# Kernel tuning notes

Hardware: AMD Instinct MI355X
Metric: run time of the kernel (lower is better)

## Reference

```python
import jax, jax.numpy as jnp
import numpy as np

N_HEADS = 16
GROUP_SIZE = 4
D_MODEL = 2048
N_GROUPS = N_HEADS // GROUP_SIZE  # 4 KV heads
HEAD_DIM = D_MODEL // N_HEADS     # 128
B, S = 2, 2048


def setup_inputs() -> dict:
    key = jax.random.key(0)
    ks = jax.random.split(key, 10)
    sd = 1.0 / np.sqrt(D_MODEL)
    inp = {
        "x": jax.random.normal(ks[0], (B, S, D_MODEL), dtype=jnp.float32),
        # per-position, per-pair rotation angles (llama-style freqs)
        "rotary_freqs": jax.random.uniform(ks[1], (S, HEAD_DIM // 2), dtype=jnp.float32) * 6.283,
        # weights stored as [in, out] so forward is x @ W + b
        "Wq": jax.random.normal(ks[2], (D_MODEL, D_MODEL), dtype=jnp.float32) * sd,
        "bq": jnp.zeros((D_MODEL,), dtype=jnp.float32),
        "Wk": jax.random.normal(ks[3], (D_MODEL, N_GROUPS * HEAD_DIM), dtype=jnp.float32) * sd,
        "bk": jnp.zeros((N_GROUPS * HEAD_DIM,), dtype=jnp.float32),
        "Wv": jax.random.normal(ks[4], (D_MODEL, N_GROUPS * HEAD_DIM), dtype=jnp.float32) * sd,
        "bv": jnp.zeros((N_GROUPS * HEAD_DIM,), dtype=jnp.float32),
        "Wo": jax.random.normal(ks[5], (D_MODEL, D_MODEL), dtype=jnp.float32) * sd,
        "bo": jnp.zeros((D_MODEL,), dtype=jnp.float32),
    }
    return inp


def _rope(t, cos, sin):
    # t: [B, S, H, head_dim]; cos/sin: [1, S, 1, head_dim//2]
    t2 = t.reshape(t.shape[:-1] + (HEAD_DIM // 2, 2))
    te, to = t2[..., 0], t2[..., 1]
    re = te * cos - to * sin
    ro = te * sin + to * cos
    return jnp.stack([re, ro], axis=-1).reshape(t.shape)


def reference(x, rotary_freqs, Wq, bq, Wk, bk, Wv, bv, Wo, bo):
    Bx, Sx, _ = x.shape
    q = (x @ Wq + bq).reshape(Bx, Sx, N_HEADS, HEAD_DIM)
    k = (x @ Wk + bk).reshape(Bx, Sx, N_GROUPS, HEAD_DIM)
    v = (x @ Wv + bv).reshape(Bx, Sx, N_GROUPS, HEAD_DIM)

    cos = jnp.cos(rotary_freqs)[None, :, None, :]
    sin = jnp.sin(rotary_freqs)[None, :, None, :]
    q = _rope(q, cos, sin)
    k = _rope(k, cos, sin)

    q = q.transpose(0, 2, 1, 3)  # [B, H, S, hd]
    k = k.transpose(0, 2, 1, 3)  # [B, G, S, hd]
    v = v.transpose(0, 2, 1, 3)  # [B, G, S, hd]

    rep = N_HEADS // N_GROUPS
    k = jnp.repeat(k, rep, axis=1)  # repeat_interleave over head dim
    v = jnp.repeat(v, rep, axis=1)

    scores = jnp.einsum("bhsd,bhtd->bhst", q, k) / jnp.sqrt(jnp.float32(HEAD_DIM))
    att = jax.nn.softmax(scores, axis=-1)
    out = jnp.einsum("bhst,bhtd->bhsd", att, v)  # [B, H, S, hd]
    out = out.transpose(0, 2, 1, 3).reshape(Bx, Sx, D_MODEL)
    return out @ Wo + bo
```

## Files before the change

### kernel.cpp

```cpp
#include <hip/hip_runtime.h>
#include <cstdint>
#include <cstddef>

#define NB 2
#define SEQ 2048
#define DMODEL 2048
#define NHEAD 16
#define HDIM 128
#define NGRP 4
#define NKV (NGRP * HDIM)
#define NQKV (DMODEL + 2 * NKV)
#define MROWS (NB * SEQ)
#define QSCALE_LOG2E 0.12751743f

typedef unsigned short u16_t;
typedef unsigned int u32_t;
typedef __bf16 bf16x8 __attribute__((ext_vector_type(8)));
typedef __bf16 bf16x4 __attribute__((ext_vector_type(4)));
typedef float f32x4 __attribute__((ext_vector_type(4)));

static __device__ __forceinline__ u16_t f2bf(float f) {
  u32_t u = __builtin_bit_cast(u32_t, f);
  u32_t r = u + 0x7FFFu + ((u >> 16) & 1u);
  return (u16_t)(r >> 16);
}


__global__ void k_cast_x(const float* __restrict__ x, u16_t* __restrict__ xb) {
  int i = blockIdx.x * 256 + threadIdx.x;
  float4 v = ((const float4*)x)[i];
  uint2 pk;
  pk.x = (u32_t)f2bf(v.x) | ((u32_t)f2bf(v.y) << 16);
  pk.y = (u32_t)f2bf(v.z) | ((u32_t)f2bf(v.w) << 16);
  ((uint2*)xb)[i] = pk;
}

__global__ void k_tables(const float* __restrict__ rf, float* __restrict__ cosT,
                         float* __restrict__ sinT) {
  int i = blockIdx.x * 256 + threadIdx.x;
  float f = rf[i];
  cosT[i] = cosf(f);
  sinT[i] = sinf(f);
}

__global__ void k_bias(const float* __restrict__ bq, const float* __restrict__ bk,
                       const float* __restrict__ bv, float* __restrict__ bqkv) {
  int i = blockIdx.x * 256 + threadIdx.x;
  float v = (i < DMODEL) ? bq[i] : (i < DMODEL + NKV ? bk[i - DMODEL] : bv[i - DMODEL - NKV]);
  bqkv[i] = v;
}

__global__ void k_transpose_cast(const float* __restrict__ W, int N,
                                 u16_t* __restrict__ Wt, int K) {
  __shared__ float tile[64][65];
  int n0 = blockIdx.x * 64, k0 = blockIdx.y * 64;
  int t = threadIdx.x;
#pragma unroll
  for (int pass = 0; pass < 4; ++pass) {
    int slot = pass * 256 + t;
    int r = slot >> 4, c4 = (slot & 15) * 4;
    float4 v = *(const float4*)(W + (size_t)(k0 + r) * N + n0 + c4);
    tile[r][c4] = v.x; tile[r][c4 + 1] = v.y; tile[r][c4 + 2] = v.z; tile[r][c4 + 3] = v.w;
  }
  __syncthreads();
  int nr = t >> 2, seg = t & 3;
  alignas(16) u16_t o[16];
#pragma unroll
  for (int kk = 0; kk < 16; ++kk) o[kk] = f2bf(tile[seg * 16 + kk][nr]);
  u16_t* dst = Wt + (size_t)(n0 + nr) * K + k0 + seg * 16;
  ((int4*)dst)[0] = ((const int4*)o)[0];
  ((int4*)dst)[1] = ((const int4*)o)[1];
}


template <int EPI>
__global__ __launch_bounds__(512, 4) void k_gemm(
    const u16_t* __restrict__ A, const u16_t* __restrict__ Bt, const float* __restrict__ bias,
    float* __restrict__ Cout, u16_t* __restrict__ Qb, u16_t* __restrict__ Kb,
    u16_t* __restrict__ Vt, const float* __restrict__ cosT, const float* __restrict__ sinT,
    int M, int N, int K) {
  __shared__ u16_t lds[32768];
  int tid = threadIdx.x;
  int wid = tid >> 6, lane = tid & 63;
  int l15 = lane & 15, l4 = lane >> 4;
  int wrow = wid >> 2, wcol = wid & 3;

  int m0 = blockIdx.y << 7, n0 = blockIdx.x << 7;

  f32x4 acc[4][2] = {};

  auto stage = [&](int t) {
    u16_t* Al = lds + (t & 1) * 8192;
    u16_t* Bl = lds + 16384 + (t & 1) * 8192;
    int kbase = t * 64;
#pragma unroll
    for (int ss = 0; ss < 2; ++ss) {
      int slot = tid + ss * 512;
      int row = slot >> 3, c = slot & 7;
      int cs = c ^ (row & 7);
      __builtin_amdgcn_global_load_lds(
          (const __attribute__((address_space(1))) u32_t*)(A + (size_t)(m0 + row) * K + kbase + cs * 8),
          (__attribute__((address_space(3))) u32_t*)(Al + slot * 8), 16, 0, 0);
      __builtin_amdgcn_global_load_lds(
          (const __attribute__((address_space(1))) u32_t*)(Bt + (size_t)(n0 + row) * K + kbase + cs * 8),
          (__attribute__((address_space(3))) u32_t*)(Bl + slot * 8), 16, 0, 0);
    }
  };

  stage(0);
  stage(1);

  const int NT = K >> 6;
  for (int t = 0; t < NT; ++t) {
    if (t == NT - 1) {
      asm volatile("s_waitcnt vmcnt(0)" ::: "memory");
    } else {
      asm volatile("s_waitcnt vmcnt(4)" ::: "memory");
    }
    __builtin_amdgcn_s_barrier();
    __builtin_amdgcn_sched_barrier(0);

    const u16_t* Acur = lds + (t & 1) * 8192;
    const u16_t* Bcur = lds + 16384 + (t & 1) * 8192;

#pragma unroll
    for (int kk = 0; kk < 2; ++kk) {
      int chunk = ((kk << 2) + l4) ^ (l15 & 7);
      bf16x8 af[4], bfr[2];
#pragma unroll
      for (int i = 0; i < 4; ++i)
        af[i] = *(const bf16x8*)(Acur + (wrow * 64 + i * 16 + l15) * 64 + chunk * 8);
#pragma unroll
      for (int j = 0; j < 2; ++j)
        bfr[j] = *(const bf16x8*)(Bcur + (wcol * 32 + j * 16 + l15) * 64 + chunk * 8);

      __builtin_amdgcn_s_setprio(1);
#pragma unroll
      for (int i = 0; i < 4; ++i)
#pragma unroll
        for (int j = 0; j < 2; ++j)
          acc[i][j] = __builtin_amdgcn_mfma_f32_16x16x32_bf16(af[i], bfr[j], acc[i][j], 0, 0, 0);
      __builtin_amdgcn_s_setprio(0);
    }

    __builtin_amdgcn_sched_barrier(0);
    __builtin_amdgcn_s_barrier();
    __builtin_amdgcn_sched_barrier(0);
    if (t + 2 < NT) stage(t + 2);
  }

  if (EPI == 0) {
#pragma unroll
    for (int j = 0; j < 2; ++j) {
      int n = n0 + wcol * 32 + j * 16 + l15;
      float bs = bias[n];
#pragma unroll
      for (int i = 0; i < 4; ++i) {
        int mbase = m0 + wrow * 64 + i * 16 + l4 * 4;
#pragma unroll
        for (int r = 0; r < 4; ++r)
          Cout[(size_t)(mbase + r) * N + n] = acc[i][j][r] + bs;
      }
    }
  } else {
    bool isV = (n0 >= DMODEL + NKV);
    bool isK = (n0 >= DMODEL) && !isV;
#pragma unroll
    for (int j = 0; j < 2; ++j) {
      int n = n0 + wcol * 32 + j * 16 + l15;
      float bs = bias[n];
      int d = n & (HDIM - 1);
      int p = d >> 1;
      bool evn = !(d & 1);
#pragma unroll
      for (int i = 0; i < 4; ++i) {
        int mbase = m0 + wrow * 64 + i * 16 + l4 * 4;
        if (isV) {
          int g = (n - DMODEL - NKV) >> 7;
          int b = mbase >> 11, s0 = mbase & (SEQ - 1);
          u16_t o[4];
#pragma unroll
          for (int r = 0; r < 4; ++r) o[r] = f2bf(acc[i][j][r] + bs);
          uint2 pk;
          pk.x = (u32_t)o[0] | ((u32_t)o[1] << 16);
          pk.y = (u32_t)o[2] | ((u32_t)o[3] << 16);
          *(uint2*)(Vt + ((size_t)(b * NGRP + g) * HDIM + d) * SEQ + s0) = pk;
        } else {
#pragma unroll
          for (int r = 0; r < 4; ++r) {
            int m = mbase + r;
            int b = m >> 11, s = m & (SEQ - 1);
            float val = acc[i][j][r] + bs;
            float pv = __shfl_xor(val, 1);
            float c = cosT[s * (HDIM / 2) + p];
            float sn = sinT[s * (HDIM / 2) + p];
            float outv = evn ? (val * c - pv * sn) : (pv * sn + val * c);
            if (isK) {
              int g = (n - DMODEL) >> 7;
              Kb[((size_t)(b * NGRP + g) * SEQ + s) * HDIM + d] = f2bf(outv);
            } else {
              int h = n >> 7;
              Qb[((size_t)(b * NHEAD + h) * SEQ + s) * HDIM + d] = f2bf(outv * QSCALE_LOG2E);
            }
          }
        }
      }
    }
  }
}


__global__ __launch_bounds__(256, 2) void k_attn(
    const u16_t* __restrict__ Qb, const u16_t* __restrict__ Kb, const u16_t* __restrict__ Vt,
    u16_t* __restrict__ attn_out) {
  __shared__ u16_t lds[32768];

  int tid = threadIdx.x, wid = tid >> 6, lane = tid & 63;
  int l15 = lane & 15, l4 = lane >> 4;
  int bh = blockIdx.y;
  int b = bh >> 4, h = bh & 15, g = h >> 2;
  int q0 = blockIdx.x * 128;
  const u16_t* Qhead = Qb + (size_t)(b * NHEAD + h) * SEQ * HDIM;
  const u16_t* Khead = Kb + (size_t)(b * NGRP + g) * SEQ * HDIM;
  const u16_t* Vhead = Vt + (size_t)(b * NGRP + g) * HDIM * SEQ;

  bf16x8 qfa[4], qfb[4];
#pragma unroll
  for (int kc = 0; kc < 4; ++kc) {
    qfa[kc] = *(const bf16x8*)(Qhead + (size_t)(q0 + wid * 32 + l15) * HDIM + kc * 32 + l4 * 8);
    qfb[kc] = *(const bf16x8*)(Qhead + (size_t)(q0 + wid * 32 + 16 + l15) * HDIM + kc * 32 + l4 * 8);
  }

  f32x4 oa[8] = {}, ob[8] = {};
  float la = 0.f, lb = 0.f;

  auto stage = [&](int kv0, int bufIdx) {
    u16_t* Kl = lds + bufIdx * 8192;
    u16_t* Vl = lds + 16384 + bufIdx * 8192;
#pragma unroll
    for (int ss = 0; ss < 4; ++ss) {
      int slot = tid + ss * 256;
      int rK = slot >> 4;
      int cK = (slot & 15) ^ ((rK & 3) | (((rK >> 3) & 1) << 2));
      __builtin_amdgcn_global_load_lds(
          (const __attribute__((address_space(1))) u32_t*)(Khead + (size_t)(kv0 + rK) * HDIM + cK * 8),
          (__attribute__((address_space(3))) u32_t*)(Kl + slot * 8), 16, 0, 0);
      int rV = slot >> 3, cV = (slot & 7) ^ (rV & 7);
      __builtin_amdgcn_global_load_lds(
          (const __attribute__((address_space(1))) u32_t*)(Vhead + (size_t)rV * SEQ + kv0 + cV * 8),
          (__attribute__((address_space(3))) u32_t*)(Vl + slot * 8), 16, 0, 0);
    }
  };

  auto qk = [&](int bufIdx, f32x4 (&Sa)[4], f32x4 (&Sb)[4]) {
    const u16_t* Kcur = lds + bufIdx * 8192;
#pragma unroll
    for (int kc = 0; kc < 4; ++kc) {
#pragma unroll
      for (int kvb = 0; kvb < 4; ++kvb) {
        int row = (l15 >> 2) * 8 + ((kvb & 1) << 2) + (l15 & 3) + ((kvb >> 1) << 5);
        int chunk = ((kc << 2) + l4) ^ (l15 & 7);
        bf16x8 kf = *(const bf16x8*)(Kcur + row * 128 + chunk * 8);
        Sa[kvb] = __builtin_amdgcn_mfma_f32_16x16x32_bf16(kf, qfa[kc], Sa[kvb], 0, 0, 0);
        Sb[kvb] = __builtin_amdgcn_mfma_f32_16x16x32_bf16(kf, qfb[kc], Sb[kvb], 0, 0, 0);
      }
    }
  };

  auto expand = [&](f32x4 (&Sa)[4], f32x4 (&Sb)[4], bf16x8 (&pfa)[2], bf16x8 (&pfb)[2]) {
    bf16x4 pa[4], pb[4];
#pragma unroll
    for (int kvb = 0; kvb < 4; ++kvb) {
#pragma unroll
      for (int r = 0; r < 4; ++r) {
        float ea = __builtin_amdgcn_exp2f(Sa[kvb][r]);
        float eb = __builtin_amdgcn_exp2f(Sb[kvb][r]);
        la += ea; lb += eb;
        pa[kvb][r] = (__bf16)ea;
        pb[kvb][r] = (__bf16)eb;
      }
    }
#pragma unroll
    for (int kc2 = 0; kc2 < 2; ++kc2) {
      uint2 alo = __builtin_bit_cast(uint2, pa[kc2 * 2]);
      uint2 ahi = __builtin_bit_cast(uint2, pa[kc2 * 2 + 1]);
      uint4 wa; wa.x = alo.x; wa.y = alo.y; wa.z = ahi.x; wa.w = ahi.y;
      pfa[kc2] = __builtin_bit_cast(bf16x8, wa);
      uint2 blo = __builtin_bit_cast(uint2, pb[kc2 * 2]);
      uint2 bhi = __builtin_bit_cast(uint2, pb[kc2 * 2 + 1]);
      uint4 wb; wb.x = blo.x; wb.y = blo.y; wb.z = bhi.x; wb.w = bhi.y;
      pfb[kc2] = __builtin_bit_cast(bf16x8, wb);
    }
  };

  auto pv = [&](int bufIdx, bf16x8 (&pfa)[2], bf16x8 (&pfb)[2]) {
    const u16_t* Vcur = lds + 16384 + bufIdx * 8192;
#pragma unroll
    for (int kc2 = 0; kc2 < 2; ++kc2) {
#pragma unroll
      for (int dcb = 0; dcb < 8; ++dcb) {
        int chunk = ((kc2 << 2) + l4) ^ (l15 & 7);
        bf16x8 vf = *(const bf16x8*)(Vcur + (dcb * 16 + l15) * 64 + chunk * 8);
        oa[dcb] = __builtin_amdgcn_mfma_f32_16x16x32_bf16(vf, pfa[kc2], oa[dcb], 0, 0, 0);
        ob[dcb] = __builtin_amdgcn_mfma_f32_16x16x32_bf16(vf, pfb[kc2], ob[dcb], 0, 0, 0);
      }
    }
  };

  auto step = [&](int t, f32x4 (&Ia)[4], f32x4 (&Ib)[4], f32x4 (&Oa)[4], f32x4 (&Ob)[4]) {
    bf16x8 pfa[2], pfb[2];
    expand(Ia, Ib, pfa, pfb);
    asm volatile("s_waitcnt vmcnt(0)" ::: "memory");
    __builtin_amdgcn_s_barrier();
    __builtin_amdgcn_sched_barrier(0);
#pragma unroll
    for (int z = 0; z < 4; ++z)
#pragma unroll
      for (int r = 0; r < 4; ++r) { Oa[z][r] = 0.f; Ob[z][r] = 0.f; }
    __builtin_amdgcn_s_setprio(1);
    pv(t & 1, pfa, pfb);
    qk((t + 1) & 1, Oa, Ob);
    __builtin_amdgcn_s_setprio(0);
    __builtin_amdgcn_sched_barrier(0);
    __builtin_amdgcn_s_barrier();
    __builtin_amdgcn_sched_barrier(0);
    if (t + 2 < SEQ / 64) stage((t + 2) * 64, t & 1);
  };

  f32x4 sA[4] = {}, sB[4] = {}, tA[4], tB[4];

  stage(0, 0);
  stage(64, 1);
  asm volatile("s_waitcnt vmcnt(8)" ::: "memory");
  __builtin_amdgcn_s_barrier();
  __builtin_amdgcn_sched_barrier(0);
  qk(0, sA, sB);

  for (int p = 0; p < 15; ++p) {
    step(2 * p, sA, sB, tA, tB);
    step(2 * p + 1, tA, tB, sA, sB);
  }
  step(30, sA, sB, tA, tB);
  {
    bf16x8 pfa[2], pfb[2];
    expand(tA, tB, pfa, pfb);
    pv(1, pfa, pfb);
  }

  la += __shfl_xor(la, 16); la += __shfl_xor(la, 32);
  lb += __shfl_xor(lb, 16); lb += __shfl_xor(lb, 32);
  float inva = 1.0f / la, invb = 1.0f / lb;

#pragma unroll
  for (int half = 0; half < 2; ++half) {
    u16_t* Owave = lds + half * 8704 + wid * 2176;
    const f32x4* oacc = half ? ob : oa;
    float inv = half ? invb : inva;
#pragma unroll
    for (int dcb = 0; dcb < 8; ++dcb) {
      bf16x4 ov;
#pragma unroll
      for (int r = 0; r < 4; ++r) ov[r] = (__bf16)(oacc[dcb][r] * inv);
      *(uint2*)(Owave + l15 * 136 + dcb * 16 + l4 * 4) = __builtin_bit_cast(uint2, ov);
    }
#pragma unroll
    for (int pass = 0; pass < 4; ++pass) {
      int rowq = pass * 4 + l4;
      int4 v = *(const int4*)(Owave + rowq * 136 + l15 * 8);
      int s = q0 + wid * 32 + half * 16 + rowq;
      *(int4*)(attn_out + ((size_t)(b * SEQ + s)) * DMODEL + h * HDIM + l15 * 8) = v;
    }
  }
}


extern "C" void kernel_launch(void* const* d_in, const int* in_sizes, int n_in,
                              void* d_out, int out_size, void* d_ws, size_t ws_size,
                              hipStream_t stream) {
  (void)in_sizes; (void)n_in; (void)out_size; (void)ws_size;
  const float* x  = (const float*)d_in[0];
  const float* rf = (const float*)d_in[1];
  const float* Wq = (const float*)d_in[2];
  const float* bq = (const float*)d_in[3];
  const float* Wk = (const float*)d_in[4];
  const float* bk = (const float*)d_in[5];
  const float* Wv = (const float*)d_in[6];
  const float* bv = (const float*)d_in[7];
  const float* Wo = (const float*)d_in[8];
  const float* bo = (const float*)d_in[9];
  float* out = (float*)d_out;

  char* ws = (char*)d_ws;
  u16_t* xb    = (u16_t*)ws;  ws += (size_t)MROWS * DMODEL * 2;
  u16_t* Wqkvt = (u16_t*)ws;  ws += (size_t)NQKV * DMODEL * 2;
  u16_t* Wot   = (u16_t*)ws;  ws += (size_t)DMODEL * DMODEL * 2;
  float* bqkv  = (float*)ws;  ws += (size_t)NQKV * 4;
  float* cosT  = (float*)ws;  ws += (size_t)SEQ * (HDIM / 2) * 4;
  float* sinT  = (float*)ws;  ws += (size_t)SEQ * (HDIM / 2) * 4;
  u16_t* Qb    = (u16_t*)ws;  ws += (size_t)NB * NHEAD * SEQ * HDIM * 2;
  u16_t* Kb    = (u16_t*)ws;  ws += (size_t)NB * NGRP * SEQ * HDIM * 2;
  u16_t* Vt    = (u16_t*)ws;  ws += (size_t)NB * NGRP * HDIM * SEQ * 2;
  u16_t* attn  = xb;

  k_cast_x<<<MROWS * DMODEL / 1024, 256, 0, stream>>>(x, xb);
  k_tables<<<SEQ * (HDIM / 2) / 256, 256, 0, stream>>>(rf, cosT, sinT);
  k_bias<<<NQKV / 256, 256, 0, stream>>>(bq, bk, bv, bqkv);

  dim3 tgq(DMODEL / 64, DMODEL / 64);
  dim3 tgk(NKV / 64, DMODEL / 64);
  k_transpose_cast<<<tgq, 256, 0, stream>>>(Wq, DMODEL, Wqkvt, DMODEL);
  k_transpose_cast<<<tgk, 256, 0, stream>>>(Wk, NKV, Wqkvt + (size_t)DMODEL * DMODEL, DMODEL);
  k_transpose_cast<<<tgk, 256, 0, stream>>>(Wv, NKV, Wqkvt + (size_t)(DMODEL + NKV) * DMODEL, DMODEL);
  k_transpose_cast<<<tgq, 256, 0, stream>>>(Wo, DMODEL, Wot, DMODEL);

  k_gemm<1><<<dim3(NQKV / 128, MROWS / 128), 512, 0, stream>>>(
      xb, Wqkvt, bqkv, nullptr, Qb, Kb, Vt, cosT, sinT, MROWS, NQKV, DMODEL);

  dim3 ga(SEQ / 128, NB * NHEAD);
  k_attn<<<ga, 256, 0, stream>>>(Qb, Kb, Vt, attn);

  k_gemm<0><<<dim3(DMODEL / 128, MROWS / 128), 512, 0, stream>>>(
      attn, Wot, bo, out, nullptr, nullptr, nullptr, nullptr, nullptr, MROWS, DMODEL, DMODEL);
}
```

Before: 186.7 us.

## Fuse prep kernels into one launch and triple-buffer K in attention

Merges the seven preprocessing launches (x cast, rope tables, bias concat, four weight transpose-casts) into a single kernel whose branch is chosen by block id, removing per-launch overhead and tail gaps between launches. In attention, K gets a third LDS buffer and is prefetched three tiles ahead, with V staged separately. The wait per step becomes vmcnt(8) instead of a full drain, so loads overlap more with compute. The row-sum accumulator is also split into a vector to shorten the dependency chain. This raises LDS use per block, which may limit occupancy, and the wait counts must match the issue order exactly.

```diff
diff --git a/kernel.cpp b/kernel.cpp
--- a/kernel.cpp
+++ b/kernel.cpp
@@ -26,35 +26,60 @@
 }
 
 
-__global__ void k_cast_x(const float* __restrict__ x, u16_t* __restrict__ xb) {
-  int i = blockIdx.x * 256 + threadIdx.x;
-  float4 v = ((const float4*)x)[i];
-  uint2 pk;
-  pk.x = (u32_t)f2bf(v.x) | ((u32_t)f2bf(v.y) << 16);
-  pk.y = (u32_t)f2bf(v.z) | ((u32_t)f2bf(v.w) << 16);
-  ((uint2*)xb)[i] = pk;
-}
-
-__global__ void k_tables(const float* __restrict__ rf, float* __restrict__ cosT,
-                         float* __restrict__ sinT) {
-  int i = blockIdx.x * 256 + threadIdx.x;
-  float f = rf[i];
-  cosT[i] = cosf(f);
-  sinT[i] = sinf(f);
-}
-
-__global__ void k_bias(const float* __restrict__ bq, const float* __restrict__ bk,
-                       const float* __restrict__ bv, float* __restrict__ bqkv) {
-  int i = blockIdx.x * 256 + threadIdx.x;
-  float v = (i < DMODEL) ? bq[i] : (i < DMODEL + NKV ? bk[i - DMODEL] : bv[i - DMODEL - NKV]);
-  bqkv[i] = v;
-}
-
-__global__ void k_transpose_cast(const float* __restrict__ W, int N,
-                                 u16_t* __restrict__ Wt, int K) {
+__global__ __launch_bounds__(256) void k_prep(
+    const float* __restrict__ x, const float* __restrict__ rf,
+    const float* __restrict__ bq, const float* __restrict__ bk, const float* __restrict__ bv,
+    const float* __restrict__ Wq, const float* __restrict__ Wk,
+    const float* __restrict__ Wv, const float* __restrict__ Wo,
+    u16_t* __restrict__ xb, float* __restrict__ cosT, float* __restrict__ sinT,
+    float* __restrict__ bqkv, u16_t* __restrict__ Wqkvt, u16_t* __restrict__ Wot) {
   __shared__ float tile[64][65];
-  int n0 = blockIdx.x * 64, k0 = blockIdx.y * 64;
-  int t = threadIdx.x;
+  int bid = blockIdx.x, t = threadIdx.x;
+
+  if (bid < 8192) {
+    int i = bid * 256 + t;
+    float4 v = ((const float4*)x)[i];
+    uint2 pk;
+    pk.x = (u32_t)f2bf(v.x) | ((u32_t)f2bf(v.y) << 16);
+    pk.y = (u32_t)f2bf(v.z) | ((u32_t)f2bf(v.w) << 16);
+    ((uint2*)xb)[i] = pk;
+    return;
+  }
+  bid -= 8192;
+  if (bid < 512) {
+    int i = bid * 256 + t;
+    float f = rf[i];
+    cosT[i] = cosf(f);
+    sinT[i] = sinf(f);
+    return;
+  }
+  bid -= 512;
+  if (bid < 12) {
+    int i = bid * 256 + t;
+    float v = (i < DMODEL) ? bq[i] : (i < DMODEL + NKV ? bk[i - DMODEL] : bv[i - DMODEL - NKV]);
+    bqkv[i] = v;
+    return;
+  }
+  bid -= 12;
+
+  const float* W; u16_t* Wt; int N, n0, k0;
+  if (bid < 1024) {
+    W = Wq; Wt = Wqkvt; N = DMODEL;
+    n0 = (bid & 31) * 64; k0 = (bid >> 5) * 64;
+  } else if (bid < 1280) {
+    int b2 = bid - 1024;
+    W = Wk; Wt = Wqkvt + (size_t)DMODEL * DMODEL; N = NKV;
+    n0 = (b2 & 7) * 64; k0 = (b2 >> 3) * 64;
+  } else if (bid < 1536) {
+    int b2 = bid - 1280;
+    W = Wv; Wt = Wqkvt + (size_t)(DMODEL + NKV) * DMODEL; N = NKV;
+    n0 = (b2 & 7) * 64; k0 = (b2 >> 3) * 64;
+  } else {
+    int b2 = bid - 1536;
+    W = Wo; Wt = Wot; N = DMODEL;
+    n0 = (b2 & 31) * 64; k0 = (b2 >> 5) * 64;
+  }
+  const int K = DMODEL;
 #pragma unroll
   for (int pass = 0; pass < 4; ++pass) {
     int slot = pass * 256 + t;
@@ -213,7 +238,7 @@
 __global__ __launch_bounds__(256, 2) void k_attn(
     const u16_t* __restrict__ Qb, const u16_t* __restrict__ Kb, const u16_t* __restrict__ Vt,
     u16_t* __restrict__ attn_out) {
-  __shared__ u16_t lds[32768];
+  __shared__ u16_t lds[40960];
 
   int tid = threadIdx.x, wid = tid >> 6, lane = tid & 63;
   int l15 = lane & 15, l4 = lane >> 4;
@@ -232,11 +257,10 @@
   }
 
   f32x4 oa[8] = {}, ob[8] = {};
-  float la = 0.f, lb = 0.f;
-
-  auto stage = [&](int kv0, int bufIdx) {
-    u16_t* Kl = lds + bufIdx * 8192;
-    u16_t* Vl = lds + 16384 + bufIdx * 8192;
+  f32x4 lav = {0.f, 0.f, 0.f, 0.f}, lbv = {0.f, 0.f, 0.f, 0.f};
+
+  auto stageK = [&](int kv0, int ks) {
+    u16_t* Kl = lds + ks * 8192;
 #pragma unroll
     for (int ss = 0; ss < 4; ++ss) {
       int slot = tid + ss * 256;
@@ -245,6 +269,13 @@
       __builtin_amdgcn_global_load_lds(
           (const __attribute__((address_space(1))) u32_t*)(Khead + (size_t)(kv0 + rK) * HDIM + cK * 8),
           (__attribute__((address_space(3))) u32_t*)(Kl + slot * 8), 16, 0, 0);
+    }
+  };
+  auto stageV = [&](int kv0, int vs) {
+    u16_t* Vl = lds + 24576 + vs * 8192;
+#pragma unroll
+    for (int ss = 0; ss < 4; ++ss) {
+      int slot = tid + ss * 256;
       int rV = slot >> 3, cV = (slot & 7) ^ (rV & 7);
       __builtin_amdgcn_global_load_lds(
           (const __attribute__((address_space(1))) u32_t*)(Vhead + (size_t)rV * SEQ + kv0 + cV * 8),
@@ -252,8 +283,8 @@
     }
   };
 
-  auto qk = [&](int bufIdx, f32x4 (&Sa)[4], f32x4 (&Sb)[4]) {
-    const u16_t* Kcur = lds + bufIdx * 8192;
+  auto qk = [&](int ks, f32x4 (&Sa)[4], f32x4 (&Sb)[4]) {
+    const u16_t* Kcur = lds + ks * 8192;
 #pragma unroll
     for (int kc = 0; kc < 4; ++kc) {
 #pragma unroll
@@ -275,7 +306,7 @@
       for (int r = 0; r < 4; ++r) {
         float ea = __builtin_amdgcn_exp2f(Sa[kvb][r]);
         float eb = __builtin_amdgcn_exp2f(Sb[kvb][r]);
-        la += ea; lb += eb;
+        lav[r] += ea; lbv[r] += eb;
         pa[kvb][r] = (__bf16)ea;
         pb[kvb][r] = (__bf16)eb;
       }
@@ -293,8 +324,8 @@
     }
   };
 
-  auto pv = [&](int bufIdx, bf16x8 (&pfa)[2], bf16x8 (&pfb)[2]) {
-    const u16_t* Vcur = lds + 16384 + bufIdx * 8192;
+  auto pv = [&](int vs, bf16x8 (&pfa)[2], bf16x8 (&pfb)[2]) {
+    const u16_t* Vcur = lds + 24576 + vs * 8192;
 #pragma unroll
     for (int kc2 = 0; kc2 < 2; ++kc2) {
 #pragma unroll
@@ -307,10 +338,17 @@
     }
   };
 
-  auto step = [&](int t, f32x4 (&Ia)[4], f32x4 (&Ib)[4], f32x4 (&Oa)[4], f32x4 (&Ob)[4]) {
+  const int NT = SEQ / 64;
+
+  auto step = [&](int t, bool last, f32x4 (&Ia)[4], f32x4 (&Ib)[4],
+                  f32x4 (&Oa)[4], f32x4 (&Ob)[4]) {
     bf16x8 pfa[2], pfb[2];
     expand(Ia, Ib, pfa, pfb);
-    asm volatile("s_waitcnt vmcnt(0)" ::: "memory");
+    if (last) {
+      asm volatile("s_waitcnt vmcnt(4)" ::: "memory");
+    } else {
+      asm volatile("s_waitcnt vmcnt(8)" ::: "memory");
+    }
     __builtin_amdgcn_s_barrier();
     __builtin_amdgcn_sched_barrier(0);
 #pragma unroll
@@ -319,34 +357,43 @@
       for (int r = 0; r < 4; ++r) { Oa[z][r] = 0.f; Ob[z][r] = 0.f; }
     __builtin_amdgcn_s_setprio(1);
     pv(t & 1, pfa, pfb);
-    qk((t + 1) & 1, Oa, Ob);
+    qk((t + 1) % 3, Oa, Ob);
     __builtin_amdgcn_s_setprio(0);
     __builtin_amdgcn_sched_barrier(0);
     __builtin_amdgcn_s_barrier();
     __builtin_amdgcn_sched_barrier(0);
-    if (t + 2 < SEQ / 64) stage((t + 2) * 64, t & 1);
+    if (t + 3 < NT) stageK((t + 3) * 64, t % 3);
+    if (t + 2 < NT) stageV((t + 2) * 64, t & 1);
   };
 
   f32x4 sA[4] = {}, sB[4] = {}, tA[4], tB[4];
 
-  stage(0, 0);
-  stage(64, 1);
+  stageK(0, 0);
+  stageK(64, 1);
+  stageV(0, 0);
   asm volatile("s_waitcnt vmcnt(8)" ::: "memory");
   __builtin_amdgcn_s_barrier();
   __builtin_amdgcn_sched_barrier(0);
+  stageK(128, 2);
+  stageV(64, 1);
   qk(0, sA, sB);
 
   for (int p = 0; p < 15; ++p) {
-    step(2 * p, sA, sB, tA, tB);
-    step(2 * p + 1, tA, tB, sA, sB);
-  }
-  step(30, sA, sB, tA, tB);
+    step(2 * p, false, sA, sB, tA, tB);
+    step(2 * p + 1, false, tA, tB, sA, sB);
+  }
+  step(30, true, sA, sB, tA, tB);
   {
     bf16x8 pfa[2], pfb[2];
     expand(tA, tB, pfa, pfb);
+    asm volatile("s_waitcnt vmcnt(0)" ::: "memory");
+    __builtin_amdgcn_s_barrier();
+    __builtin_amdgcn_sched_barrier(0);
     pv(1, pfa, pfb);
   }
 
+  float la = lav[0] + lav[1] + lav[2] + lav[3];
+  float lb = lbv[0] + lbv[1] + lbv[2] + lbv[3];
   la += __shfl_xor(la, 16); la += __shfl_xor(la, 32);
   lb += __shfl_xor(lb, 16); lb += __shfl_xor(lb, 32);
   float inva = 1.0f / la, invb = 1.0f / lb;
@@ -402,16 +449,8 @@
   u16_t* Vt    = (u16_t*)ws;  ws += (size_t)NB * NGRP * HDIM * SEQ * 2;
   u16_t* attn  = xb;
 
-  k_cast_x<<<MROWS * DMODEL / 1024, 256, 0, stream>>>(x, xb);
-  k_tables<<<SEQ * (HDIM / 2) / 256, 256, 0, stream>>>(rf, cosT, sinT);
-  k_bias<<<NQKV / 256, 256, 0, stream>>>(bq, bk, bv, bqkv);
-
-  dim3 tgq(DMODEL / 64, DMODEL / 64);
-  dim3 tgk(NKV / 64, DMODEL / 64);
-  k_transpose_cast<<<tgq, 256, 0, stream>>>(Wq, DMODEL, Wqkvt, DMODEL);
-  k_transpose_cast<<<tgk, 256, 0, stream>>>(Wk, NKV, Wqkvt + (size_t)DMODEL * DMODEL, DMODEL);
-  k_transpose_cast<<<tgk, 256, 0, stream>>>(Wv, NKV, Wqkvt + (size_t)(DMODEL + NKV) * DMODEL, DMODEL);
-  k_transpose_cast<<<tgq, 256, 0, stream>>>(Wo, DMODEL, Wot, DMODEL);
+  k_prep<<<11276, 256, 0, stream>>>(x, rf, bq, bk, bv, Wq, Wk, Wv, Wo,
+                                    xb, cosT, sinT, bqkv, Wqkvt, Wot);
 
   k_gemm<1><<<dim3(NQKV / 128, MROWS / 128), 512, 0, stream>>>(
       xb, Wqkvt, bqkv, nullptr, Qb, Kb, Vt, cosT, sinT, MROWS, NQKV, DMODEL);
```

Result: faster. 177.3 us (-5.0%).
